# Optimization experiments

Measured on AMD Instinct MI355X. Metric: run time of the kernel, lower is better.

## Reference

```python
import jax, jax.numpy as jnp
from jax import lax
import numpy as np

DN = ('NCHW', 'OIHW', 'NCHW')

def conv2d(x, w, b, pad):
    y = lax.conv_general_dilated(x, w, (1, 1), [(pad, pad), (pad, pad)], dimension_numbers=DN)
    return y + b[None, :, None, None]

def setup_inputs() -> dict:
    key = jax.random.key(0)
    ks = jax.random.split(key, 20)
    B, C, H, W = 2, 256, 64, 64
    d = {}
    d['Fl'] = jax.random.normal(ks[0], (B, C, H, W), dtype=jnp.float32)
    d['Fv'] = jax.random.normal(ks[1], (B, C, H, W), dtype=jnp.float32)
    s3 = 1.0 / np.sqrt(C * 9)
    s1 = 1.0 / np.sqrt(C)
    names3 = ['Wqs', 'Wks', 'Wvs', 'Wqc', 'Wkc', 'Wvc']
    for i, n in enumerate(names3):
        d[n] = jax.random.normal(ks[2 + 2 * i], (C, C, 3, 3), dtype=jnp.float32) * s3
        d['b' + n[1:]] = jax.random.normal(ks[3 + 2 * i], (C,), dtype=jnp.float32) * 0.01
    d['Wgs'] = jax.random.normal(ks[14], (C, C, 1, 1), dtype=jnp.float32) * s1
    d['bgs'] = jax.random.normal(ks[15], (C,), dtype=jnp.float32) * 0.01
    d['Wfuse'] = jax.random.normal(ks[16], (C, 2 * C, 1, 1), dtype=jnp.float32) * (1.0 / np.sqrt(2 * C))
    d['bfuse'] = jax.random.normal(ks[17], (C,), dtype=jnp.float32) * 0.01
    return d

def reference(Fl, Fv, Wqs, bqs, Wks, bks, Wvs, bvs, Wqc, bqc, Wkc, bkc, Wvc, bvc, Wgs, bgs, Wfuse, bfuse):
    b, c, h, w = Fl.shape
    hw = h * w
    # --- self branch (on Fl) ---
    Qs = conv2d(Fl, Wqs, bqs, 1).reshape(b, c, hw)
    Ks = conv2d(Fl, Wks, bks, 1).reshape(b, c, hw)
    Vs = conv2d(Fl, Wvs, bvs, 1).reshape(b, c, hw)
    multi_s = jnp.einsum('bjk,bjq->bkq', Qs, Ks)          # [b, hw, hw]
    multi_s = jax.nn.softmax(multi_s, axis=1)              # softmax over dim=1 (as in torch code)
    Gs = jnp.einsum('bik,bjk->bij', multi_s, Vs)           # [b, hw, c]
    Gs = Gs.reshape(b, c, h, w)                            # raw reshape, faithful to torch
    Gs = conv2d(Gs, Wgs, bgs, 0) + Fl
    # --- cross branch (Q from Fl, K/V from Fv) ---
    Qc = conv2d(Fl, Wqc, bqc, 1).reshape(b, c, hw)
    Kc = conv2d(Fv, Wkc, bkc, 1).reshape(b, c, hw)
    Vc = conv2d(Fv, Wvc, bvc, 1).reshape(b, c, hw)
    multi_c = jnp.einsum('bjk,bjq->bkq', Qc, Kc)
    multi_c = jax.nn.softmax(multi_c, axis=1)
    Gc = jnp.einsum('bik,bjk->bij', multi_c, Vc)
    Gc = Gc.reshape(b, c, h, w)
    Gc = conv2d(Gc, Wgs, bgs, 0) + Fv                      # note: original uses Gs_conv for both branches
    out = conv2d(jnp.concatenate([Gs, Gc], axis=1), Wfuse, bfuse, 0)
    return out
```

## Files before the change

### kernel.cpp

```cpp
#include <hip/hip_runtime.h>

typedef __bf16 bf16x4 __attribute__((ext_vector_type(4)));
typedef __bf16 bf16x8 __attribute__((ext_vector_type(8)));
typedef float  f32x4  __attribute__((ext_vector_type(4)));

#define HWSZ 4096
#define CCH  256
#define LOG2E 1.44269504088896340736f

__device__ __forceinline__ float exp2_fast(float x) {
#if __has_builtin(__builtin_amdgcn_exp2f)
  return __builtin_amdgcn_exp2f(x);
#else
  return exp2f(x);
#endif
}

__device__ __forceinline__ void stage16(const __bf16* g, __bf16* ldsBase) {
#if __has_builtin(__builtin_amdgcn_global_load_lds)
  __builtin_amdgcn_global_load_lds(
      (const __attribute__((address_space(1))) void*)g,
      (__attribute__((address_space(3))) void*)ldsBase, 16, 0, 0);
#else
  int lane = threadIdx.x & 63;
  *(bf16x8*)(ldsBase + lane * 8) = *(const bf16x8*)g;
#endif
}

#define SWZ_STAGE(lane) ((((lane) & 3) ^ (((lane) >> 3) & 3)) * 8)
#define SWZ_READ(quad, lane) ((((quad) ^ (((lane) >> 1) & 3))) * 8)

__global__ __launch_bounds__(256)
void gemm_conv(const __bf16* __restrict__ AL, const __bf16* __restrict__ AV,
               const __bf16* __restrict__ Cc,
               __bf16* __restrict__ qst, __bf16* __restrict__ kst,
               __bf16* __restrict__ vs,  __bf16* __restrict__ qct,
               __bf16* __restrict__ kct, __bf16* __restrict__ vc,
               const float* __restrict__ bqs, const float* __restrict__ bks,
               const float* __restrict__ bvs, const float* __restrict__ bqc,
               const float* __restrict__ bkc, const float* __restrict__ bvc)
{
  __shared__ __align__(16) __bf16 smem[8192];
  __bf16* As = smem;
  __bf16* Bs = smem + 4096;

  const int tid  = threadIdx.x;
  const int lane = tid & 63;
  const int w    = tid >> 6;
  const int wm   = (w >> 1) * 64;
  const int wn   = (w & 1) * 64;
  const int z    = blockIdx.z;
  const int by   = blockIdx.y;
  const int bn   = blockIdx.x * 128;
  const int K    = 2304;

  const bool isL = (by < 8);
  const int bm = (isL ? by : by - 8) * 128;
  const __bf16* Ab = isL ? AL : AV;
  const __bf16* Bb = Cc + (long)((isL ? 0 : 2) + z) * 9437184;

  f32x4 acc[4][4] = {};
  const int srow = lane >> 2;
  const int skc  = SWZ_STAGE(lane);
  const int quad = lane >> 4, l15 = lane & 15;
  const int rdo  = SWZ_READ(quad, lane);

  for (int k0 = 0; k0 < K; k0 += 32) {
#pragma unroll
    for (int j = 0; j < 2; ++j) {
      int rbase = w * 32 + j * 16;
      stage16(Ab + (long)(bm + rbase + srow) * K + k0 + skc, As + rbase * 32);
    }
#pragma unroll
    for (int j = 0; j < 2; ++j) {
      int rbase = w * 32 + j * 16;
      stage16(Bb + (long)(bn + rbase + srow) * K + k0 + skc, Bs + rbase * 32);
    }
    __syncthreads();
    bf16x8 af[4], bfr[4];
#pragma unroll
    for (int t = 0; t < 4; ++t)
      af[t] = *(const bf16x8*)(As + (wm + t * 16 + l15) * 32 + rdo);
#pragma unroll
    for (int t = 0; t < 4; ++t)
      bfr[t] = *(const bf16x8*)(Bs + (wn + t * 16 + l15) * 32 + rdo);
#pragma unroll
    for (int mt = 0; mt < 4; ++mt)
#pragma unroll
      for (int nt = 0; nt < 4; ++nt)
        acc[mt][nt] = __builtin_amdgcn_mfma_f32_16x16x32_bf16(af[mt], bfr[nt], acc[mt][nt], 0, 0, 0);
    __syncthreads();
  }

#pragma unroll
  for (int mt = 0; mt < 4; ++mt) {
#pragma unroll
    for (int nt = 0; nt < 4; ++nt) {
#pragma unroll
      for (int r = 0; r < 4; ++r) {
        int m = bm + wm + mt * 16 + quad * 4 + r;
        int n = bn + wn + nt * 16 + l15;
        int g = m >> 8, mm = m & 255;
        const float* bias; __bf16* op; bool vlay;
        if (isL) {
          bias = (g == 0) ? bqs : (g == 1) ? bks : (g == 2) ? bvs : bqc;
          op   = (g == 0) ? qst : (g == 1) ? kst : (g == 2) ? vs  : qct;
          vlay = (g == 2);
        } else {
          bias = g ? bvc : bkc;
          op   = g ? vc  : kct;
          vlay = (g == 1);
        }
        float vv = acc[mt][nt][r] + bias[mm];
        if (vlay) op[(long)z * 1048576 + (long)mm * HWSZ + n] = (__bf16)vv;
        else      op[(long)z * 1048576 + (long)n * CCH + mm] = (__bf16)vv;
      }
    }
  }
}

__global__ __launch_bounds__(256)
void qk_stats(const __bf16* __restrict__ qs, const __bf16* __restrict__ qc,
              const __bf16* __restrict__ ks, const __bf16* __restrict__ kc,
              float* __restrict__ pm, float* __restrict__ pl)
{
  __shared__ __align__(16) __bf16 Kres[64 * 260];
  __shared__ float wm_[4][64], wl_[4][64];

  const int tid = threadIdx.x, lane = tid & 63, w = tid >> 6;
  const int quad = lane >> 4, l15 = lane & 15;
  const int lid = blockIdx.x;
  const int g = lid & 3;
  const int z = g & 1, br = g >> 1;
  const int ih = (lid >> 2) & 1;
  const int qb = (lid >> 3) * 64;
  const __bf16* Qt = (br ? qc : qs) + (long)z * 1048576;
  const __bf16* Kt = (br ? kc : ks) + (long)z * 1048576;

  for (int idx = tid; idx < 2048; idx += 256) {
    int r = idx >> 5, c8 = (idx & 31) * 8;
    *(bf16x8*)(Kres + r * 260 + c8) = *(const bf16x8*)(Kt + (long)(qb + r) * 256 + c8);
  }
  __syncthreads();

  float rm[4], rl[4];
#pragma unroll
  for (int nt = 0; nt < 4; ++nt) { rm[nt] = -3.0e38f; rl[nt] = 0.f; }

  for (int it = 0; it < 8; ++it) {
    const int i0 = ih * 2048 + it * 256 + w * 64;
    f32x4 accS[4][4] = {};
#pragma unroll
    for (int cs = 0; cs < 256; cs += 32) {
      bf16x8 a[4], b[4];
#pragma unroll
      for (int mt = 0; mt < 4; ++mt)
        a[mt] = *(const bf16x8*)(Qt + (long)(i0 + mt * 16 + l15) * 256 + cs + quad * 8);
#pragma unroll
      for (int nt = 0; nt < 4; ++nt)
        b[nt] = *(const bf16x8*)(Kres + (nt * 16 + l15) * 260 + cs + quad * 8);
#pragma unroll
      for (int mt = 0; mt < 4; ++mt)
#pragma unroll
        for (int nt = 0; nt < 4; ++nt)
          accS[mt][nt] = __builtin_amdgcn_mfma_f32_16x16x32_bf16(a[mt], b[nt], accS[mt][nt], 0, 0, 0);
    }
#pragma unroll
    for (int nt = 0; nt < 4; ++nt) {
      float mx = -3.0e38f;
#pragma unroll
      for (int mt = 0; mt < 4; ++mt)
#pragma unroll
        for (int r = 0; r < 4; ++r) mx = fmaxf(mx, accS[mt][nt][r]);
      float sl = 0.f;
#pragma unroll
      for (int mt = 0; mt < 4; ++mt)
#pragma unroll
        for (int r = 0; r < 4; ++r) sl += exp2_fast((accS[mt][nt][r] - mx) * LOG2E);
#pragma unroll
      for (int d = 16; d <= 32; d <<= 1) {
        float om = __shfl_xor(mx, d, 64);
        float ol = __shfl_xor(sl, d, 64);
        float nm = fmaxf(mx, om);
        sl = sl * exp2_fast((mx - nm) * LOG2E) + ol * exp2_fast((om - nm) * LOG2E);
        mx = nm;
      }
      float nm = fmaxf(rm[nt], mx);
      rl[nt] = rl[nt] * exp2_fast((rm[nt] - nm) * LOG2E) + sl * exp2_fast((mx - nm) * LOG2E);
      rm[nt] = nm;
    }
  }
  if (lane < 16) {
#pragma unroll
    for (int nt = 0; nt < 4; ++nt) { wm_[w][nt * 16 + lane] = rm[nt]; wl_[w][nt * 16 + lane] = rl[nt]; }
  }
  __syncthreads();
  if (tid < 64) {
    float m = -3.0e38f;
#pragma unroll
    for (int ww = 0; ww < 4; ++ww) m = fmaxf(m, wm_[ww][tid]);
    float l = 0.f;
#pragma unroll
    for (int ww = 0; ww < 4; ++ww)
      l += wl_[ww][tid] * exp2_fast((wm_[ww][tid] - m) * LOG2E);
    long o = ((long)ih * 4 + br * 2 + z) * 4096 + qb + tid;
    pm[o] = m;
    pl[o] = l;
  }
}

__global__ void stats_combine2(const float* __restrict__ pm, const float* __restrict__ pl,
                               float* __restrict__ mst, float* __restrict__ lst) {
  int q = blockIdx.x * 256 + threadIdx.x;
  int zbr = blockIdx.y;
  float m0 = pm[(long)zbr * 4096 + q],        l0 = pl[(long)zbr * 4096 + q];
  float m1 = pm[(long)(4 + zbr) * 4096 + q],  l1 = pl[(long)(4 + zbr) * 4096 + q];
  float m = fmaxf(m0, m1);
  float l = l0 * exp2_fast((m0 - m) * LOG2E) + l1 * exp2_fast((m1 - m) * LOG2E);
  mst[(long)zbr * 4096 + q] = m;
  lst[(long)zbr * 4096 + q] = 1.0f / l;
}

__global__ __launch_bounds__(512, 4)
void fused_pv(const __bf16* __restrict__ qs, const __bf16* __restrict__ qc,
              const __bf16* __restrict__ ks, const __bf16* __restrict__ kc,
              const __bf16* __restrict__ vs, const __bf16* __restrict__ vc,
              const float* __restrict__ mst, const float* __restrict__ lst,
              float* __restrict__ gacc)
{
  __shared__ __align__(16) __bf16 Qres[64 * 260];
  __shared__ __align__(16) __bf16 Pl[64 * 132];

  const int tid = threadIdx.x, lane = tid & 63, w = tid >> 6;
  const int quad = lane >> 4, l15 = lane & 15;
  const int lid = blockIdx.x;
  const int g   = lid & 7;
  const int zbr = g >> 1;
  const int qh  = g & 1;
  const int bi  = (lid >> 3) * 64;
  const int br = zbr >> 1, z = zbr & 1;
  const __bf16* Qt = (br ? qc : qs) + (long)z * 1048576;
  const __bf16* Kt = (br ? kc : ks) + (long)z * 1048576;
  const __bf16* Vv = (br ? vc : vs) + (long)z * 1048576;
  const float* msp = mst + (long)zbr * 4096;
  const float* lsp = lst + (long)zbr * 4096;
  float* go = gacc + ((long)qh * 4 + zbr) * 1048576;

  for (int idx = tid; idx < 2048; idx += 512) {
    int r = idx >> 5, c8 = (idx & 31) * 8;
    *(bf16x8*)(Qres + r * 260 + c8) = *(const bf16x8*)(Qt + (long)(bi + r) * 256 + c8);
  }
  __syncthreads();

  f32x4 accO[4][2] = {};
  const int q0 = qh * 2048;
  const __bf16* Vl0 = Vv + (long)(w * 32 + l15) * 4096 + quad * 8;
  const __bf16* Vl1 = Vl0 + (long)16 * 4096;

  for (int qc0 = q0; qc0 < q0 + 2048; qc0 += 128) {
    f32x4 accS[4] = {};
    const __bf16* Kl = Kt + (long)(qc0 + w * 16 + l15) * 256 + quad * 8;
#pragma unroll
    for (int cs = 0; cs < 256; cs += 32) {
      bf16x8 aq[4];
      bf16x8 bk = *(const bf16x8*)(Kl + cs);
#pragma unroll
      for (int mt = 0; mt < 4; ++mt)
        aq[mt] = *(const bf16x8*)(Qres + (mt * 16 + l15) * 260 + cs + quad * 8);
#pragma unroll
      for (int mt = 0; mt < 4; ++mt)
        accS[mt] = __builtin_amdgcn_mfma_f32_16x16x32_bf16(aq[mt], bk, accS[mt], 0, 0, 0);
    }
    __syncthreads();
    {
      int q = w * 16 + l15;
      float mq = msp[qc0 + q], lq = lsp[qc0 + q];
#pragma unroll
      for (int mt = 0; mt < 4; ++mt)
#pragma unroll
        for (int r = 0; r < 4; ++r) {
          int i = mt * 16 + quad * 4 + r;
          Pl[i * 132 + q] = (__bf16)(exp2_fast((accS[mt][r] - mq) * LOG2E) * lq);
        }
    }
    __syncthreads();
#pragma unroll
    for (int qs0 = 0; qs0 < 128; qs0 += 32) {
      bf16x8 ap[4], bv0, bv1;
      bv0 = *(const bf16x8*)(Vl0 + qc0 + qs0);
      bv1 = *(const bf16x8*)(Vl1 + qc0 + qs0);
#pragma unroll
      for (int mt = 0; mt < 4; ++mt)
        ap[mt] = *(const bf16x8*)(Pl + (mt * 16 + l15) * 132 + qs0 + quad * 8);
#pragma unroll
      for (int mt = 0; mt < 4; ++mt) {
        accO[mt][0] = __builtin_amdgcn_mfma_f32_16x16x32_bf16(ap[mt], bv0, accO[mt][0], 0, 0, 0);
        accO[mt][1] = __builtin_amdgcn_mfma_f32_16x16x32_bf16(ap[mt], bv1, accO[mt][1], 0, 0, 0);
      }
    }
  }
#pragma unroll
  for (int mt = 0; mt < 4; ++mt)
#pragma unroll
    for (int nt = 0; nt < 2; ++nt)
#pragma unroll
      for (int r = 0; r < 4; ++r) {
        int i = mt * 16 + quad * 4 + r;
        int j = w * 32 + nt * 16 + l15;
        go[(long)(bi + i) * 256 + j] = accO[mt][nt][r];
      }
}

__global__ __launch_bounds__(256)
void gsum_reshape(const float* __restrict__ ga, __bf16* __restrict__ gt) {
  __shared__ __bf16 lds[64 * 260];
  const int t = threadIdx.x, lane = t & 63, w = t >> 6;
  const int zbr = blockIdx.z;
  const int v   = blockIdx.y;
  const int jg  = blockIdx.x;
  const float* g0 = ga + (long)zbr * 1048576;
  const float* g1 = g0 + 4194304;
  for (int ci0 = 0; ci0 < 256; ci0 += 4) {
    int ci = ci0 + w;
    long src = (long)(ci * 16 + v) * 256 + jg * 64 + lane;
    lds[lane * 260 + ci] = (__bf16)(g0[src] + g1[src]);
  }
  __syncthreads();
  __bf16* out = gt + (long)zbr * 1048576 + ((long)v * 256 + jg * 64) * 256;
#pragma unroll
  for (int pp = 0; pp < 8; ++pp) {
    int idx = pp * 256 + t;
    int row = idx >> 5, c8 = (idx & 31) * 8;
    *(bf16x8*)(out + (long)row * 256 + c8) = *(const bf16x8*)(lds + row * 260 + c8);
  }
}

__global__ __launch_bounds__(256)
void wcomb(const float* __restrict__ Wgs, const float* __restrict__ bgs,
           const float* __restrict__ Wfu, const float* __restrict__ bfu,
           __bf16* __restrict__ WT, float* __restrict__ biasT)
{
  const int co = blockIdx.x, t = threadIdx.x;
  const float* wrow = Wfu + (long)co * 512;
  float accs = 0.f, accc = 0.f;
  for (int c = 0; c < 256; ++c) {
    float gv = Wgs[(long)c * 256 + t];
    accs = fmaf(wrow[c], gv, accs);
    accc = fmaf(wrow[c + 256], gv, accc);
  }
  __bf16* o = WT + (long)co * 1024;
  o[t]       = (__bf16)accs;
  o[256 + t] = (__bf16)accc;
  o[512 + t] = (__bf16)wrow[t];
  o[768 + t] = (__bf16)wrow[256 + t];
  __shared__ float red[256];
  red[t] = (wrow[t] + wrow[t + 256]) * bgs[t];
  __syncthreads();
  for (int s = 128; s > 0; s >>= 1) {
    if (t < s) red[t] += red[t + s];
    __syncthreads();
  }
  if (t == 0) biasT[co] = bfu[co] + red[0];
}

__global__ __launch_bounds__(256)
void tail_gemm(const __bf16* __restrict__ WT, const __bf16* __restrict__ GTS,
               const __bf16* __restrict__ Xt, const float* __restrict__ biasT,
               float* __restrict__ out)
{
  __shared__ __align__(16) __bf16 smem[8192];
  __bf16* As = smem;
  __bf16* Bs = smem + 4096;

  const int tid  = threadIdx.x;
  const int lane = tid & 63;
  const int w    = tid >> 6;
  const int wm   = (w >> 1) * 64;
  const int wn   = (w & 1) * 64;
  const int z    = blockIdx.z;
  const int bm   = blockIdx.y * 128;
  const int bn   = blockIdx.x * 128;

  const __bf16* Bsel[4] = {
    GTS + (long)z * 1048576, GTS + (long)(2 + z) * 1048576,
    Xt  + (long)z * 1048576, Xt  + (long)(2 + z) * 1048576
  };

  f32x4 acc[4][4] = {};
  const int srow = lane >> 2;
  const int skc  = SWZ_STAGE(lane);
  const int quad = lane >> 4, l15 = lane & 15;
  const int rdo  = SWZ_READ(quad, lane);

  for (int k0 = 0; k0 < 1024; k0 += 32) {
    const __bf16* Bb = Bsel[k0 >> 8];
    const int kk = k0 & 255;
#pragma unroll
    for (int j = 0; j < 2; ++j) {
      int rbase = w * 32 + j * 16;
      stage16(WT + (long)(bm + rbase + srow) * 1024 + k0 + skc, As + rbase * 32);
    }
#pragma unroll
    for (int j = 0; j < 2; ++j) {
      int rbase = w * 32 + j * 16;
      stage16(Bb + (long)(bn + rbase + srow) * 256 + kk + skc, Bs + rbase * 32);
    }
    __syncthreads();
    bf16x8 af[4], bfr[4];
#pragma unroll
    for (int t = 0; t < 4; ++t)
      af[t] = *(const bf16x8*)(As + (wm + t * 16 + l15) * 32 + rdo);
#pragma unroll
    for (int t = 0; t < 4; ++t)
      bfr[t] = *(const bf16x8*)(Bs + (wn + t * 16 + l15) * 32 + rdo);
#pragma unroll
    for (int mt = 0; mt < 4; ++mt)
#pragma unroll
      for (int nt = 0; nt < 4; ++nt)
        acc[mt][nt] = __builtin_amdgcn_mfma_f32_16x16x32_bf16(af[mt], bfr[nt], acc[mt][nt], 0, 0, 0);
    __syncthreads();
  }

#pragma unroll
  for (int mt = 0; mt < 4; ++mt)
#pragma unroll
    for (int nt = 0; nt < 4; ++nt)
#pragma unroll
      for (int r = 0; r < 4; ++r) {
        int m = bm + wm + mt * 16 + quad * 4 + r;
        int n = bn + wn + nt * 16 + l15;
        out[((long)z * 256 + m) * HWSZ + n] = acc[mt][nt][r] + biasT[m];
      }
}

__global__ void transpose_cvt(const float* __restrict__ F0, const float* __restrict__ F1,
                              __bf16* __restrict__ Xt) {
  __shared__ float tile[32][33];
  int img = blockIdx.z;
  const float* src = (img < 2 ? F0 : F1) + (long)(img & 1) * (CCH * HWSZ);
  __bf16* dst = Xt + (long)img * (HWSZ * CCH);
  int p0 = blockIdx.x * 32, c0 = blockIdx.y * 32;
  int tx = threadIdx.x, ty = threadIdx.y;
#pragma unroll
  for (int j = 0; j < 32; j += 8)
    tile[ty + j][tx] = src[(long)(c0 + ty + j) * HWSZ + p0 + tx];
  __syncthreads();
#pragma unroll
  for (int j = 0; j < 32; j += 8)
    dst[(long)(p0 + ty + j) * CCH + c0 + tx] = (__bf16)tile[tx][ty + j];
}

__global__ void im2col_k(const __bf16* __restrict__ Xt, __bf16* __restrict__ Cc) {
  int img = blockIdx.y;
  int e = blockIdx.x * 256 + threadIdx.x;
  int p = e / 288;
  int c8 = e - p * 288;
  int t = c8 >> 5;
  int ci0 = (c8 & 31) * 8;
  int dy = t / 3 - 1, dx = t - (t / 3) * 3 - 1;
  int y = p >> 6, x = p & 63;
  int yy = y + dy, xx = x + dx;
  const __bf16* src = Xt + (long)img * (HWSZ * CCH);
  __bf16* dst = Cc + (long)img * 9437184 + (long)p * 2304 + t * 256 + ci0;
  uint4 v = make_uint4(0u, 0u, 0u, 0u);
  if ((unsigned)yy < 64u && (unsigned)xx < 64u)
    v = *(const uint4*)(src + (long)(yy * 64 + xx) * CCH + ci0);
  *(uint4*)dst = v;
}

struct W6 { const float* w[6]; };
__global__ void repack_w3(W6 wp, __bf16* __restrict__ AL, __bf16* __restrict__ AV) {
  int zi = blockIdx.y;
  int e = blockIdx.x * 256 + threadIdx.x;
  int co = e / 2304;
  int rem = e - co * 2304;
  int t = rem >> 8, ci = rem & 255;
  float v = wp.w[zi][(long)co * 2304 + ci * 9 + t];
  __bf16* dst = (zi < 4) ? (AL + (long)zi * 256 * 2304) : (AV + (long)(zi - 4) * 256 * 2304);
  dst[(long)co * 2304 + rem] = (__bf16)v;
}

extern "C" void kernel_launch(void* const* d_in, const int* in_sizes, int n_in,
                              void* d_out, int out_size, void* d_ws, size_t ws_size,
                              hipStream_t stream) {
  const float* Fl  = (const float*)d_in[0];
  const float* Fv  = (const float*)d_in[1];
  const float* Wqs = (const float*)d_in[2];  const float* bqs = (const float*)d_in[3];
  const float* Wks = (const float*)d_in[4];  const float* bks = (const float*)d_in[5];
  const float* Wvs = (const float*)d_in[6];  const float* bvs = (const float*)d_in[7];
  const float* Wqc = (const float*)d_in[8];  const float* bqc = (const float*)d_in[9];
  const float* Wkc = (const float*)d_in[10]; const float* bkc = (const float*)d_in[11];
  const float* Wvc = (const float*)d_in[12]; const float* bvc = (const float*)d_in[13];
  const float* Wgs = (const float*)d_in[14]; const float* bgs = (const float*)d_in[15];
  const float* Wfu = (const float*)d_in[16]; const float* bfu = (const float*)d_in[17];

  char* ws = (char*)d_ws;
  size_t off = 0;
  auto take = [&](size_t bytes) -> void* {
    void* p = ws + off; off = (off + bytes + 255) & ~(size_t)255; return p;
  };
  __bf16* QST  = (__bf16*)take(4194304);
  __bf16* KST  = (__bf16*)take(4194304);
  __bf16* QCT  = (__bf16*)take(4194304);
  __bf16* KCT  = (__bf16*)take(4194304);
  __bf16* VS   = (__bf16*)take(4194304);
  __bf16* VC   = (__bf16*)take(4194304);
  __bf16* GTS  = (__bf16*)take(8388608);
  __bf16* AL   = (__bf16*)take(4718592);
  __bf16* AV   = (__bf16*)take(2359296);
  __bf16* WT   = (__bf16*)take(524288);
  float*  BT   = (float*)take(1024);
  float*  MST  = (float*)take(65536);
  float*  LST  = (float*)take(65536);
  float*  PM   = (float*)take(131072);
  float*  PL   = (float*)take(131072);
  __bf16* Xt   = (__bf16*)take(8388608);
  size_t ovl = off;
  __bf16* Cc = (__bf16*)take(75497472);
  size_t needConv = off;
  float* GACC = (float*)(ws + ovl);
  size_t needAttn = ovl + 33554432;
  size_t need = needConv > needAttn ? needConv : needAttn;
  if (ws_size < need) return;

  transpose_cvt<<<dim3(128, 8, 4), dim3(32, 8), 0, stream>>>(Fl, Fv, Xt);
  im2col_k<<<dim3(4608, 4), 256, 0, stream>>>(Xt, Cc);
  W6 wp; wp.w[0]=Wqs; wp.w[1]=Wks; wp.w[2]=Wvs; wp.w[3]=Wqc; wp.w[4]=Wkc; wp.w[5]=Wvc;
  repack_w3<<<dim3(2304, 6), 256, 0, stream>>>(wp, AL, AV);
  wcomb<<<dim3(256), 256, 0, stream>>>(Wgs, bgs, Wfu, bfu, WT, BT);

  gemm_conv<<<dim3(32, 12, 2), 256, 0, stream>>>(
      AL, AV, Cc, QST, KST, VS, QCT, KCT, VC,
      bqs, bks, bvs, bqc, bkc, bvc);

  qk_stats<<<dim3(512), 256, 0, stream>>>(QST, QCT, KST, KCT, PM, PL);
  stats_combine2<<<dim3(16, 4), 256, 0, stream>>>(PM, PL, MST, LST);

  fused_pv<<<dim3(512), 512, 0, stream>>>(
      QST, QCT, KST, KCT, VS, VC, MST, LST, GACC);

  gsum_reshape<<<dim3(4, 16, 4), 256, 0, stream>>>(GACC, GTS);

  tail_gemm<<<dim3(32, 2, 2), 256, 0, stream>>>(WT, GTS, Xt, BT, (float*)d_out);
}
```

Baseline: 455.4 us.

## Double key tile per iteration in fused_pv and prefetch V before barriers

The fused P·V attention kernel now handles 256 keys per outer iteration instead of 128, with each wave computing two 16-column score tiles. This halves the number of barrier pairs and loop overheads. The first two V fragments and the softmax statistics are loaded before the barrier so their global latency overlaps the LDS sync. The __syncthreads calls are replaced by an explicit lgkmcnt wait plus s_barrier, which does not wait on outstanding global loads. In exchange the P LDS buffer nearly doubles and register pressure rises, which may hurt occupancy under launch_bounds(512,4).

```diff
diff --git a/kernel.cpp b/kernel.cpp
--- a/kernel.cpp
+++ b/kernel.cpp
@@ -14,6 +14,11 @@
 #else
   return exp2f(x);
 #endif
+}
+
+__device__ __forceinline__ void bar_lgkm() {
+  asm volatile("s_waitcnt lgkmcnt(0)" ::: "memory");
+  __builtin_amdgcn_s_barrier();
 }
 
 __device__ __forceinline__ void stage16(const __bf16* g, __bf16* ldsBase) {
@@ -229,7 +234,7 @@
               float* __restrict__ gacc)
 {
   __shared__ __align__(16) __bf16 Qres[64 * 260];
-  __shared__ __align__(16) __bf16 Pl[64 * 132];
+  __shared__ __align__(16) __bf16 Pl[64 * 260];
 
   const int tid = threadIdx.x, lane = tid & 63, w = tid >> 6;
   const int quad = lane >> 4, l15 = lane & 15;
@@ -257,41 +262,56 @@
   const __bf16* Vl0 = Vv + (long)(w * 32 + l15) * 4096 + quad * 8;
   const __bf16* Vl1 = Vl0 + (long)16 * 4096;
 
-  for (int qc0 = q0; qc0 < q0 + 2048; qc0 += 128) {
-    f32x4 accS[4] = {};
-    const __bf16* Kl = Kt + (long)(qc0 + w * 16 + l15) * 256 + quad * 8;
+  for (int qc0 = q0; qc0 < q0 + 2048; qc0 += 256) {
+    f32x4 accS[4][2] = {};
+    const __bf16* Kl0 = Kt + (long)(qc0 + w * 32 + l15) * 256 + quad * 8;
+    const __bf16* Kl1 = Kl0 + (long)16 * 256;
 #pragma unroll
     for (int cs = 0; cs < 256; cs += 32) {
       bf16x8 aq[4];
-      bf16x8 bk = *(const bf16x8*)(Kl + cs);
+      bf16x8 bk0 = *(const bf16x8*)(Kl0 + cs);
+      bf16x8 bk1 = *(const bf16x8*)(Kl1 + cs);
 #pragma unroll
       for (int mt = 0; mt < 4; ++mt)
         aq[mt] = *(const bf16x8*)(Qres + (mt * 16 + l15) * 260 + cs + quad * 8);
 #pragma unroll
-      for (int mt = 0; mt < 4; ++mt)
-        accS[mt] = __builtin_amdgcn_mfma_f32_16x16x32_bf16(aq[mt], bk, accS[mt], 0, 0, 0);
-    }
-    __syncthreads();
-    {
-      int q = w * 16 + l15;
-      float mq = msp[qc0 + q], lq = lsp[qc0 + q];
+      for (int mt = 0; mt < 4; ++mt) {
+        accS[mt][0] = __builtin_amdgcn_mfma_f32_16x16x32_bf16(aq[mt], bk0, accS[mt][0], 0, 0, 0);
+        accS[mt][1] = __builtin_amdgcn_mfma_f32_16x16x32_bf16(aq[mt], bk1, accS[mt][1], 0, 0, 0);
+      }
+    }
+    float mq0 = msp[qc0 + w * 32 + l15],      lq0 = lsp[qc0 + w * 32 + l15];
+    float mq1 = msp[qc0 + w * 32 + 16 + l15], lq1 = lsp[qc0 + w * 32 + 16 + l15];
+    bf16x8 pv00 = *(const bf16x8*)(Vl0 + qc0);
+    bf16x8 pv01 = *(const bf16x8*)(Vl1 + qc0);
+    bf16x8 pv10 = *(const bf16x8*)(Vl0 + qc0 + 32);
+    bf16x8 pv11 = *(const bf16x8*)(Vl1 + qc0 + 32);
+    bar_lgkm();
+#pragma unroll
+    for (int nt = 0; nt < 2; ++nt) {
+      int q = w * 32 + nt * 16 + l15;
+      float mq = nt ? mq1 : mq0, lq = nt ? lq1 : lq0;
 #pragma unroll
       for (int mt = 0; mt < 4; ++mt)
 #pragma unroll
         for (int r = 0; r < 4; ++r) {
           int i = mt * 16 + quad * 4 + r;
-          Pl[i * 132 + q] = (__bf16)(exp2_fast((accS[mt][r] - mq) * LOG2E) * lq);
+          Pl[i * 260 + q] = (__bf16)(exp2_fast((accS[mt][nt][r] - mq) * LOG2E) * lq);
         }
     }
-    __syncthreads();
-#pragma unroll
-    for (int qs0 = 0; qs0 < 128; qs0 += 32) {
+    bar_lgkm();
+#pragma unroll
+    for (int qs0 = 0; qs0 < 256; qs0 += 32) {
       bf16x8 ap[4], bv0, bv1;
-      bv0 = *(const bf16x8*)(Vl0 + qc0 + qs0);
-      bv1 = *(const bf16x8*)(Vl1 + qc0 + qs0);
-#pragma unroll
-      for (int mt = 0; mt < 4; ++mt)
-        ap[mt] = *(const bf16x8*)(Pl + (mt * 16 + l15) * 132 + qs0 + quad * 8);
+      if (qs0 == 0)       { bv0 = pv00; bv1 = pv01; }
+      else if (qs0 == 32) { bv0 = pv10; bv1 = pv11; }
+      else {
+        bv0 = *(const bf16x8*)(Vl0 + qc0 + qs0);
+        bv1 = *(const bf16x8*)(Vl1 + qc0 + qs0);
+      }
+#pragma unroll
+      for (int mt = 0; mt < 4; ++mt)
+        ap[mt] = *(const bf16x8*)(Pl + (mt * 16 + l15) * 260 + qs0 + quad * 8);
 #pragma unroll
       for (int mt = 0; mt < 4; ++mt) {
         accO[mt][0] = __builtin_amdgcn_mfma_f32_16x16x32_bf16(ap[mt], bv0, accO[mt][0], 0, 0, 0);
```

New measurement: 441.0 us. -3.2%, faster.

## Rewrite fused_pv with 32x32 MFMA and register-resident P via lane shuffles

Applied to the files above, without the earlier changes.

The fused P·V kernel moves from 16x16x32 to 32x32x16 bf16 MFMA. It computes S transposed so the softmax probabilities can be packed and exchanged between lane halves with shuffles, which removes the LDS staging of P and its two barriers per tile. The query range is now split four ways across wave pairs in a block rather than two ways across blocks, so the grid halves and the partial-output buffer doubles. gsum_reshape now sums four partials. The trade-off is higher register pressure (launch bounds drop from 4 to 2 blocks per CU), fewer blocks in flight, and more global traffic for the partial accumulators.

```diff
diff --git a/kernel.cpp b/kernel.cpp
--- a/kernel.cpp
+++ b/kernel.cpp
@@ -3,6 +3,8 @@
 typedef __bf16 bf16x4 __attribute__((ext_vector_type(4)));
 typedef __bf16 bf16x8 __attribute__((ext_vector_type(8)));
 typedef float  f32x4  __attribute__((ext_vector_type(4)));
+typedef float  f32x16 __attribute__((ext_vector_type(16)));
+typedef unsigned u32x4 __attribute__((ext_vector_type(4)));
 
 #define HWSZ 4096
 #define CCH  256
@@ -14,6 +16,12 @@
 #else
   return exp2f(x);
 #endif
+}
+
+__device__ __forceinline__ unsigned pack2bf(float a, float b) {
+  unsigned short ua = __builtin_bit_cast(unsigned short, (__bf16)a);
+  unsigned short ub = __builtin_bit_cast(unsigned short, (__bf16)b);
+  return (unsigned)ua | ((unsigned)ub << 16);
 }
 
 __device__ __forceinline__ void stage16(const __bf16* g, __bf16* ldsBase) {
@@ -221,94 +229,102 @@
   lst[(long)zbr * 4096 + q] = 1.0f / l;
 }
 
-__global__ __launch_bounds__(512, 4)
+__global__ __launch_bounds__(512, 2)
 void fused_pv(const __bf16* __restrict__ qs, const __bf16* __restrict__ qc,
               const __bf16* __restrict__ ks, const __bf16* __restrict__ kc,
               const __bf16* __restrict__ vs, const __bf16* __restrict__ vc,
               const float* __restrict__ mst, const float* __restrict__ lst,
               float* __restrict__ gacc)
 {
-  __shared__ __align__(16) __bf16 Qres[64 * 260];
-  __shared__ __align__(16) __bf16 Pl[64 * 132];
+  __shared__ __align__(16) __bf16 Qlds[64 * 264];
 
   const int tid = threadIdx.x, lane = tid & 63, w = tid >> 6;
-  const int quad = lane >> 4, l15 = lane & 15;
+  const int l31 = lane & 31, hi = lane >> 5;
   const int lid = blockIdx.x;
-  const int g   = lid & 7;
-  const int zbr = g >> 1;
-  const int qh  = g & 1;
-  const int bi  = (lid >> 3) * 64;
+  const int zbr = lid & 3;
+  const int bi  = (lid >> 2) * 64;
   const int br = zbr >> 1, z = zbr & 1;
+  const int islice = (w & 1) * 32;
+  const int qg = w >> 1;
   const __bf16* Qt = (br ? qc : qs) + (long)z * 1048576;
   const __bf16* Kt = (br ? kc : ks) + (long)z * 1048576;
   const __bf16* Vv = (br ? vc : vs) + (long)z * 1048576;
   const float* msp = mst + (long)zbr * 4096;
   const float* lsp = lst + (long)zbr * 4096;
-  float* go = gacc + ((long)qh * 4 + zbr) * 1048576;
+  float* go = gacc + ((long)qg * 4 + zbr) * 1048576;
 
   for (int idx = tid; idx < 2048; idx += 512) {
     int r = idx >> 5, c8 = (idx & 31) * 8;
-    *(bf16x8*)(Qres + r * 260 + c8) = *(const bf16x8*)(Qt + (long)(bi + r) * 256 + c8);
+    *(bf16x8*)(Qlds + r * 264 + c8) = *(const bf16x8*)(Qt + (long)(bi + r) * 256 + c8);
   }
   __syncthreads();
 
-  f32x4 accO[4][2] = {};
-  const int q0 = qh * 2048;
-  const __bf16* Vl0 = Vv + (long)(w * 32 + l15) * 4096 + quad * 8;
-  const __bf16* Vl1 = Vl0 + (long)16 * 4096;
-
-  for (int qc0 = q0; qc0 < q0 + 2048; qc0 += 128) {
-    f32x4 accS[4] = {};
-    const __bf16* Kl = Kt + (long)(qc0 + w * 16 + l15) * 256 + quad * 8;
-#pragma unroll
-    for (int cs = 0; cs < 256; cs += 32) {
-      bf16x8 aq[4];
-      bf16x8 bk = *(const bf16x8*)(Kl + cs);
-#pragma unroll
-      for (int mt = 0; mt < 4; ++mt)
-        aq[mt] = *(const bf16x8*)(Qres + (mt * 16 + l15) * 260 + cs + quad * 8);
-#pragma unroll
-      for (int mt = 0; mt < 4; ++mt)
-        accS[mt] = __builtin_amdgcn_mfma_f32_16x16x32_bf16(aq[mt], bk, accS[mt], 0, 0, 0);
-    }
-    __syncthreads();
-    {
-      int q = w * 16 + l15;
-      float mq = msp[qc0 + q], lq = lsp[qc0 + q];
-#pragma unroll
-      for (int mt = 0; mt < 4; ++mt)
-#pragma unroll
-        for (int r = 0; r < 4; ++r) {
-          int i = mt * 16 + quad * 4 + r;
-          Pl[i * 132 + q] = (__bf16)(exp2_fast((accS[mt][r] - mq) * LOG2E) * lq);
-        }
-    }
-    __syncthreads();
-#pragma unroll
-    for (int qs0 = 0; qs0 < 128; qs0 += 32) {
-      bf16x8 ap[4], bv0, bv1;
-      bv0 = *(const bf16x8*)(Vl0 + qc0 + qs0);
-      bv1 = *(const bf16x8*)(Vl1 + qc0 + qs0);
-#pragma unroll
-      for (int mt = 0; mt < 4; ++mt)
-        ap[mt] = *(const bf16x8*)(Pl + (mt * 16 + l15) * 132 + qs0 + quad * 8);
-#pragma unroll
-      for (int mt = 0; mt < 4; ++mt) {
-        accO[mt][0] = __builtin_amdgcn_mfma_f32_16x16x32_bf16(ap[mt], bv0, accO[mt][0], 0, 0, 0);
-        accO[mt][1] = __builtin_amdgcn_mfma_f32_16x16x32_bf16(ap[mt], bv1, accO[mt][1], 0, 0, 0);
+  f32x16 accO[8] = {};
+
+  const __bf16* Qrow = Qlds + (islice + l31) * 264 + hi * 8;
+
+  for (int step = 0; step < 16; ++step) {
+    const int qb = qg * 1024 + step * 64;
+    f32x16 accST0 = {}, accST1 = {};
+    const __bf16* K0 = Kt + (long)(qb + l31) * 256 + hi * 8;
+    const __bf16* K1 = K0 + 32 * 256;
+#pragma unroll
+    for (int cs = 0; cs < 16; ++cs) {
+      bf16x8 bq  = *(const bf16x8*)(Qrow + cs * 16);
+      bf16x8 ka0 = *(const bf16x8*)(K0 + cs * 16);
+      bf16x8 ka1 = *(const bf16x8*)(K1 + cs * 16);
+      accST0 = __builtin_amdgcn_mfma_f32_32x32x16_bf16(ka0, bq, accST0, 0, 0, 0);
+      accST1 = __builtin_amdgcn_mfma_f32_32x32x16_bf16(ka1, bq, accST1, 0, 0, 0);
+    }
+    bf16x8 pa[4];
+#pragma unroll
+    for (int qt = 0; qt < 2; ++qt) {
+      f32x16 a = qt ? accST1 : accST0;
+      unsigned pk[8], sh[8];
+#pragma unroll
+      for (int rr = 0; rr < 4; ++rr) {
+        f32x4 mq = *(const f32x4*)(msp + qb + qt * 32 + rr * 8 + 4 * hi);
+        f32x4 lq = *(const f32x4*)(lsp + qb + qt * 32 + rr * 8 + 4 * hi);
+        float p0 = exp2_fast((a[rr * 4 + 0] - mq[0]) * LOG2E) * lq[0];
+        float p1 = exp2_fast((a[rr * 4 + 1] - mq[1]) * LOG2E) * lq[1];
+        float p2 = exp2_fast((a[rr * 4 + 2] - mq[2]) * LOG2E) * lq[2];
+        float p3 = exp2_fast((a[rr * 4 + 3] - mq[3]) * LOG2E) * lq[3];
+        pk[rr * 2 + 0] = pack2bf(p0, p1);
+        pk[rr * 2 + 1] = pack2bf(p2, p3);
       }
-    }
-  }
-#pragma unroll
-  for (int mt = 0; mt < 4; ++mt)
-#pragma unroll
-    for (int nt = 0; nt < 2; ++nt)
-#pragma unroll
-      for (int r = 0; r < 4; ++r) {
-        int i = mt * 16 + quad * 4 + r;
-        int j = w * 32 + nt * 16 + l15;
-        go[(long)(bi + i) * 256 + j] = accO[mt][nt][r];
+#pragma unroll
+      for (int j = 0; j < 8; ++j) sh[j] = __shfl_xor(pk[j], 32, 64);
+#pragma unroll
+      for (int kb = 0; kb < 2; ++kb) {
+        u32x4 dd;
+        dd[0] = hi ? sh[4 * kb + 2] : pk[4 * kb + 0];
+        dd[1] = hi ? sh[4 * kb + 3] : pk[4 * kb + 1];
+        dd[2] = hi ? pk[4 * kb + 2] : sh[4 * kb + 0];
+        dd[3] = hi ? pk[4 * kb + 3] : sh[4 * kb + 1];
+        pa[qt * 2 + kb] = __builtin_bit_cast(bf16x8, dd);
       }
+    }
+#pragma unroll
+    for (int jt = 0; jt < 8; ++jt) {
+      const __bf16* Vb = Vv + (long)(jt * 32 + l31) * 4096 + qb + hi * 8;
+      bf16x8 bv0 = *(const bf16x8*)(Vb);
+      bf16x8 bv1 = *(const bf16x8*)(Vb + 16);
+      bf16x8 bv2 = *(const bf16x8*)(Vb + 32);
+      bf16x8 bv3 = *(const bf16x8*)(Vb + 48);
+      accO[jt] = __builtin_amdgcn_mfma_f32_32x32x16_bf16(pa[0], bv0, accO[jt], 0, 0, 0);
+      accO[jt] = __builtin_amdgcn_mfma_f32_32x32x16_bf16(pa[1], bv1, accO[jt], 0, 0, 0);
+      accO[jt] = __builtin_amdgcn_mfma_f32_32x32x16_bf16(pa[2], bv2, accO[jt], 0, 0, 0);
+      accO[jt] = __builtin_amdgcn_mfma_f32_32x32x16_bf16(pa[3], bv3, accO[jt], 0, 0, 0);
+    }
+  }
+#pragma unroll
+  for (int jt = 0; jt < 8; ++jt)
+#pragma unroll
+    for (int reg = 0; reg < 16; ++reg) {
+      int i = bi + islice + (reg & 3) + 8 * (reg >> 2) + 4 * hi;
+      int j = jt * 32 + l31;
+      go[(long)i * 256 + j] = accO[jt][reg];
+    }
 }
 
 __global__ __launch_bounds__(256)
@@ -319,11 +335,11 @@
   const int v   = blockIdx.y;
   const int jg  = blockIdx.x;
   const float* g0 = ga + (long)zbr * 1048576;
-  const float* g1 = g0 + 4194304;
   for (int ci0 = 0; ci0 < 256; ci0 += 4) {
     int ci = ci0 + w;
     long src = (long)(ci * 16 + v) * 256 + jg * 64 + lane;
-    lds[lane * 260 + ci] = (__bf16)(g0[src] + g1[src]);
+    float s = g0[src] + g0[src + 4194304] + g0[src + 8388608] + g0[src + 12582912];
+    lds[lane * 260 + ci] = (__bf16)s;
   }
   __syncthreads();
   __bf16* out = gt + (long)zbr * 1048576 + ((long)v * 256 + jg * 64) * 256;
@@ -519,7 +535,7 @@
   __bf16* Cc = (__bf16*)take(75497472);
   size_t needConv = off;
   float* GACC = (float*)(ws + ovl);
-  size_t needAttn = ovl + 33554432;
+  size_t needAttn = ovl + 67108864;
   size_t need = needConv > needAttn ? needConv : needAttn;
   if (ws_size < need) return;
 
@@ -536,7 +552,7 @@
   qk_stats<<<dim3(512), 256, 0, stream>>>(QST, QCT, KST, KCT, PM, PL);
   stats_combine2<<<dim3(16, 4), 256, 0, stream>>>(PM, PL, MST, LST);
 
-  fused_pv<<<dim3(512), 512, 0, stream>>>(
+  fused_pv<<<dim3(256), 512, 0, stream>>>(
       QST, QCT, KST, KCT, VS, VC, MST, LST, GACC);
 
   gsum_reshape<<<dim3(4, 16, 4), 256, 0, stream>>>(GACC, GTS);
```

Result: slower. 575.9 us (+26.5%).
